# Optimization experiments

Measured on AMD Instinct MI355X. Metric: run time of the kernel, lower is better.

The kernel has to match this reference:

```python
import jax, jax.numpy as jnp
import numpy as np

_LEVELS = jnp.array([-4, -2, -1, 0, 1, 2, 4], dtype=jnp.int32)  # shift-quant 7-value grid 'A'

B, S = 1, 512
IN_F, OUT_F = 4096, 16384
BLOCK = 64
NUM_BLOCKS = (IN_F + BLOCK - 1) // BLOCK  # 64


def setup_inputs() -> dict:
    key = jax.random.key(0)
    k1, k2, k3, k4 = jax.random.split(key, 4)
    x = jax.random.normal(k1, (B, S, IN_F), dtype=jnp.float32)
    idx = jax.random.randint(k2, (OUT_F, IN_F), 0, 7)
    q_weight = _LEVELS[idx]  # int32 values in {-4,-2,-1,0,1,2,4}
    scales = (jax.random.uniform(k3, (OUT_F, NUM_BLOCKS), dtype=jnp.float32) * 0.05 + 0.001).astype(jnp.float16)
    bias = (jax.random.normal(k4, (OUT_F,), dtype=jnp.float32) * 0.02).astype(jnp.float16)
    return {"x": x, "q_weight": q_weight, "scales": scales, "bias": bias, "block_size": BLOCK}


def reference(x, q_weight, scales, bias, block_size):
    # shift_matmul: dequantize blockwise-scaled power-of-two int8 weights, then GEMM.
    out_f, in_f = q_weight.shape
    # broadcast per-block fp16 scales along the in_features axis (handles padding block)
    w_scale = jnp.repeat(scales.astype(jnp.float32), block_size, axis=1)[:, :in_f]  # [out, in]
    w = q_weight.astype(jnp.float32) * w_scale  # [out, in]
    out = jnp.einsum("bsi,oi->bso", x, w)
    out = out + bias.astype(out.dtype)
    return out.astype(x.dtype)
```

## Files before the change

kernel.cpp:

```cpp
#include <hip/hip_runtime.h>
#include <hip/hip_bf16.h>
#include <stdint.h>


#define MM 512
#define NN 16384
#define KK 4096
#define BN 64
#define BK 128
#define NKB (KK / BK)

typedef __bf16 bf16x8 __attribute__((ext_vector_type(8)));
typedef float floatx4 __attribute__((ext_vector_type(4)));

__device__ __forceinline__ void barrier_nodrain() {
    asm volatile("s_waitcnt lgkmcnt(0)\n\ts_barrier" ::: "memory");
}

__device__ __forceinline__ unsigned int pk_bf16_rtn(float lo, float hi) {
    __hip_bfloat162 h = __float22bfloat162_rn(float2{lo, hi});
    return *reinterpret_cast<unsigned int*>(&h);
}

__device__ __forceinline__ uint4 deq8(const int4 q0, const int4 q1, const float s) {
    uint4 u;
    u.x = pk_bf16_rtn((float)q0.x * s, (float)q0.y * s);
    u.y = pk_bf16_rtn((float)q0.z * s, (float)q0.w * s);
    u.z = pk_bf16_rtn((float)q1.x * s, (float)q1.y * s);
    u.w = pk_bf16_rtn((float)q1.z * s, (float)q1.w * s);
    return u;
}

__global__ __launch_bounds__(256) void pack_x(const float* __restrict__ x,
                                              unsigned short* __restrict__ xp) {
    const int t    = blockIdx.x * 256 + threadIdx.x;
    const int lane = t & 63;
    const int mt   = (t >> 6) & 31;
    const int ks   = (t >> 11) & 3;
    const int kb   = t >> 13;
    const int m    = mt * 16 + (lane & 15);
    const int k    = kb * 128 + ks * 32 + (lane >> 4) * 8;
    const float* px = x + (size_t)m * KK + k;
    const float4 a = *(const float4*)px;
    const float4 b = *(const float4*)(px + 4);
    uint4 o;
    o.x = pk_bf16_rtn(a.x, a.y);
    o.y = pk_bf16_rtn(a.z, a.w);
    o.z = pk_bf16_rtn(b.x, b.y);
    o.w = pk_bf16_rtn(b.z, b.w);
    *(uint4*)(xp + (size_t)t * 8) = o;
}

template <bool PRE>
__global__ __launch_bounds__(512, 4) void qlin_gemm(
    const float* __restrict__ xf,
    const unsigned short* __restrict__ xp,
    const int* __restrict__ qw,
    const float* __restrict__ scales,
    const float* __restrict__ bias,
    float* __restrict__ out)
{
    __shared__ unsigned short sB[2][BN * BK];

    const int t    = threadIdx.x;
    const int lane = t & 63;
    const int w    = t >> 6;
    const int ln   = lane & 15;
    const int quad = lane >> 4;
    const int h    = blockIdx.x & 1;
    const int n0   = (blockIdx.x >> 1) * BN;

    const int r    = t >> 4;
    const int oct  = t & 15;
    const int ksp  = oct >> 2;
    const int jp   = r >> 4;
    const int ldst = (((oct & 3) << 4) | (r & 15)) ^ (ksp << 1);
    const int woff = ((ksp * 4 + jp) * 64 + ldst) * 8;
    const int* qp0   = qw + (size_t)(n0 + r) * KK + oct * 8;
    const int* qp1   = qp0 + (size_t)32 * KK;
    const float* sp0 = scales + (size_t)(n0 + r) * 64 + (oct >> 3);
    const float* sp1 = sp0 + 32 * 64;

    floatx4 acc[2][4];
#pragma unroll
    for (int i = 0; i < 2; ++i)
#pragma unroll
        for (int j = 0; j < 4; ++j)
            acc[i][j] = (floatx4)0.0f;

    int4 qa0 = *(const int4*)(qp0);
    int4 qa1 = *(const int4*)(qp0 + 4);
    int4 qb0 = *(const int4*)(qp1);
    int4 qb1 = *(const int4*)(qp1 + 4);
    float sa = sp0[0];
    float sc = sp1[0];

    bf16x8 a[4][2];

    for (int kb = 0; kb < NKB; ++kb) {
        unsigned short* sbuf = sB[kb & 1];

        if constexpr (PRE) {
            const unsigned short* xpb = xp + (size_t)kb * (4 * 32 * 64 * 8);
#pragma unroll
            for (int ks = 0; ks < 4; ++ks) {
                const unsigned short* ap =
                    xpb + (size_t)((ks * 32 + h * 16 + w * 2) * 64 + lane) * 8;
                a[ks][0] = *(const bf16x8*)(ap);
                a[ks][1] = *(const bf16x8*)(ap + 512);
            }
        }

        {
            uint4 u0 = deq8(qa0, qa1, sa);
            uint4 u1 = deq8(qb0, qb1, sc);
            *(uint4*)(sbuf + woff)        = u0;
            *(uint4*)(sbuf + woff + 1024) = u1;
        }

        if (kb + 1 < NKB) {
            qa0 = *(const int4*)(qp0 + (size_t)(kb + 1) * BK);
            qa1 = *(const int4*)(qp0 + (size_t)(kb + 1) * BK + 4);
            qb0 = *(const int4*)(qp1 + (size_t)(kb + 1) * BK);
            qb1 = *(const int4*)(qp1 + (size_t)(kb + 1) * BK + 4);
            sa = sp0[(size_t)(kb + 1) * 2];
            sc = sp1[(size_t)(kb + 1) * 2];
        }

        barrier_nodrain();

#pragma unroll
        for (int ks = 0; ks < 4; ++ks) {
            bf16x8 a0, a1;
            if constexpr (PRE) {
                a0 = a[ks][0];
                a1 = a[ks][1];
            } else {
                const int k = kb * BK + ks * 32 + quad * 8;
#pragma unroll
                for (int i = 0; i < 2; ++i) {
                    const float* px =
                        xf + (size_t)(h * 256 + w * 32 + i * 16 + ln) * KK + k;
                    const float4 f0 = *(const float4*)px;
                    const float4 f1 = *(const float4*)(px + 4);
                    uint4 ua;
                    ua.x = pk_bf16_rtn(f0.x, f0.y);
                    ua.y = pk_bf16_rtn(f0.z, f0.w);
                    ua.z = pk_bf16_rtn(f1.x, f1.y);
                    ua.w = pk_bf16_rtn(f1.z, f1.w);
                    if (i == 0) a0 = *(bf16x8*)&ua; else a1 = *(bf16x8*)&ua;
                }
            }
            const int sl = lane ^ (ks << 1);
#pragma unroll
            for (int jj = 0; jj < 4; jj += 2) {
                bf16x8 b0 = *(const bf16x8*)(sbuf + ((ks * 4 + jj) * 64 + sl) * 8);
                bf16x8 b1 = *(const bf16x8*)(sbuf + ((ks * 4 + jj + 1) * 64 + sl) * 8);
                acc[0][jj]     = __builtin_amdgcn_mfma_f32_16x16x32_bf16(a0, b0, acc[0][jj], 0, 0, 0);
                acc[1][jj]     = __builtin_amdgcn_mfma_f32_16x16x32_bf16(a1, b0, acc[1][jj], 0, 0, 0);
                acc[0][jj + 1] = __builtin_amdgcn_mfma_f32_16x16x32_bf16(a0, b1, acc[0][jj + 1], 0, 0, 0);
                acc[1][jj + 1] = __builtin_amdgcn_mfma_f32_16x16x32_bf16(a1, b1, acc[1][jj + 1], 0, 0, 0);
            }
        }
    }

#pragma unroll
    for (int j = 0; j < 4; ++j) {
        const int n = n0 + j * 16 + ln;
        const float bv = bias[n];
#pragma unroll
        for (int i = 0; i < 2; ++i) {
            const int mbase = h * 256 + w * 32 + i * 16 + quad * 4;
#pragma unroll
            for (int rr = 0; rr < 4; ++rr)
                out[(size_t)(mbase + rr) * NN + n] = acc[i][j][rr] + bv;
        }
    }
}

extern "C" void kernel_launch(void* const* d_in, const int* in_sizes, int n_in,
                              void* d_out, int out_size, void* d_ws, size_t ws_size,
                              hipStream_t stream) {
    const float* x    = (const float*)d_in[0];
    const int* qw     = (const int*)d_in[1];
    const float* scl  = (const float*)d_in[2];
    const float* bias = (const float*)d_in[3];
    float* out        = (float*)d_out;

    dim3 grid(NN / BN * 2);
    dim3 block(512);

    if (ws_size >= (size_t)MM * KK * sizeof(unsigned short)) {
        unsigned short* xp = (unsigned short*)d_ws;
        pack_x<<<dim3(MM * KK / (256 * 8)), dim3(256), 0, stream>>>(x, xp);
        qlin_gemm<true><<<grid, block, 0, stream>>>(x, xp, qw, scl, bias, out);
    } else {
        qlin_gemm<false><<<grid, block, 0, stream>>>(x, nullptr, qw, scl, bias, out);
    }
}
```

Baseline: 442.2 us.

## Software-pipeline dequant, weight prefetch and A loads across K-blocks with per-phase barriers

Restructures the main loop into a prologue-staged ping-pong pipeline. The dequantized weight tile for the next K-block is written while the current tile is consumed, weights are prefetched two blocks ahead, and the A fragments for the next block are loaded right after each phase's MFMAs. Each of the four k-phases now issues all its LDS reads before a barrier and raises wave priority around the MFMA group. The aim is to hide global-load and dequant latency behind matrix math, at the cost of four barriers per K-block instead of one and more registers live at once.

After: 437.4 us. No clear change (-1.1%).

```diff
diff --git a/kernel.cpp b/kernel.cpp
--- a/kernel.cpp
+++ b/kernel.cpp
@@ -97,46 +97,69 @@
 
     bf16x8 a[4][2];
 
+    {
+        uint4 u0 = deq8(qa0, qa1, sa);
+        uint4 u1 = deq8(qb0, qb1, sc);
+        *(uint4*)(sB[0] + woff)        = u0;
+        *(uint4*)(sB[0] + woff + 1024) = u1;
+    }
+    qa0 = *(const int4*)(qp0 + BK);
+    qa1 = *(const int4*)(qp0 + BK + 4);
+    qb0 = *(const int4*)(qp1 + BK);
+    qb1 = *(const int4*)(qp1 + BK + 4);
+    sa = sp0[2];
+    sc = sp1[2];
+    if constexpr (PRE) {
+#pragma unroll
+        for (int p = 0; p < 4; ++p) {
+            const unsigned short* ap =
+                xp + (size_t)((p * 32 + h * 16 + w * 2) * 64 + lane) * 8;
+            a[p][0] = *(const bf16x8*)(ap);
+            a[p][1] = *(const bf16x8*)(ap + 512);
+        }
+    }
+    barrier_nodrain();
+
     for (int kb = 0; kb < NKB; ++kb) {
-        unsigned short* sbuf = sB[kb & 1];
-
-        if constexpr (PRE) {
-            const unsigned short* xpb = xp + (size_t)kb * (4 * 32 * 64 * 8);
-#pragma unroll
-            for (int ks = 0; ks < 4; ++ks) {
-                const unsigned short* ap =
-                    xpb + (size_t)((ks * 32 + h * 16 + w * 2) * 64 + lane) * 8;
-                a[ks][0] = *(const bf16x8*)(ap);
-                a[ks][1] = *(const bf16x8*)(ap + 512);
-            }
-        }
-
-        {
-            uint4 u0 = deq8(qa0, qa1, sa);
-            uint4 u1 = deq8(qb0, qb1, sc);
-            *(uint4*)(sbuf + woff)        = u0;
-            *(uint4*)(sbuf + woff + 1024) = u1;
-        }
-
-        if (kb + 1 < NKB) {
-            qa0 = *(const int4*)(qp0 + (size_t)(kb + 1) * BK);
-            qa1 = *(const int4*)(qp0 + (size_t)(kb + 1) * BK + 4);
-            qb0 = *(const int4*)(qp1 + (size_t)(kb + 1) * BK);
-            qb1 = *(const int4*)(qp1 + (size_t)(kb + 1) * BK + 4);
-            sa = sp0[(size_t)(kb + 1) * 2];
-            sc = sp1[(size_t)(kb + 1) * 2];
-        }
-
-        barrier_nodrain();
-
-#pragma unroll
-        for (int ks = 0; ks < 4; ++ks) {
+        const int cur = kb & 1;
+        const unsigned short* sbR = sB[cur];
+        unsigned short* sbW       = sB[cur ^ 1];
+        const bool stage = (kb + 1 < NKB);
+
+#pragma unroll
+        for (int p = 0; p < 4; ++p) {
+            if (p == 0 && stage) {
+                uint4 u0 = deq8(qa0, qa1, sa);
+                *(uint4*)(sbW + woff) = u0;
+            }
+            if (p == 1 && stage) {
+                uint4 u1 = deq8(qb0, qb1, sc);
+                *(uint4*)(sbW + woff + 1024) = u1;
+            }
+            if (p == 3 && kb + 2 < NKB) {
+                qa0 = *(const int4*)(qp0 + (size_t)(kb + 2) * BK);
+                qa1 = *(const int4*)(qp0 + (size_t)(kb + 2) * BK + 4);
+                qb0 = *(const int4*)(qp1 + (size_t)(kb + 2) * BK);
+                qb1 = *(const int4*)(qp1 + (size_t)(kb + 2) * BK + 4);
+                sa = sp0[(size_t)(kb + 2) * 2];
+                sc = sp1[(size_t)(kb + 2) * 2];
+            }
+
+            const int sl = lane ^ (p << 1);
+            bf16x8 b0 = *(const bf16x8*)(sbR + ((p * 4 + 0) * 64 + sl) * 8);
+            bf16x8 b1 = *(const bf16x8*)(sbR + ((p * 4 + 1) * 64 + sl) * 8);
+            bf16x8 b2 = *(const bf16x8*)(sbR + ((p * 4 + 2) * 64 + sl) * 8);
+            bf16x8 b3 = *(const bf16x8*)(sbR + ((p * 4 + 3) * 64 + sl) * 8);
+
+            barrier_nodrain();
+            __builtin_amdgcn_sched_barrier(0);
+
             bf16x8 a0, a1;
             if constexpr (PRE) {
-                a0 = a[ks][0];
-                a1 = a[ks][1];
+                a0 = a[p][0];
+                a1 = a[p][1];
             } else {
-                const int k = kb * BK + ks * 32 + quad * 8;
+                const int k = kb * BK + p * 32 + quad * 8;
 #pragma unroll
                 for (int i = 0; i < 2; ++i) {
                     const float* px =
@@ -151,15 +174,26 @@
                     if (i == 0) a0 = *(bf16x8*)&ua; else a1 = *(bf16x8*)&ua;
                 }
             }
-            const int sl = lane ^ (ks << 1);
-#pragma unroll
-            for (int jj = 0; jj < 4; jj += 2) {
-                bf16x8 b0 = *(const bf16x8*)(sbuf + ((ks * 4 + jj) * 64 + sl) * 8);
-                bf16x8 b1 = *(const bf16x8*)(sbuf + ((ks * 4 + jj + 1) * 64 + sl) * 8);
-                acc[0][jj]     = __builtin_amdgcn_mfma_f32_16x16x32_bf16(a0, b0, acc[0][jj], 0, 0, 0);
-                acc[1][jj]     = __builtin_amdgcn_mfma_f32_16x16x32_bf16(a1, b0, acc[1][jj], 0, 0, 0);
-                acc[0][jj + 1] = __builtin_amdgcn_mfma_f32_16x16x32_bf16(a0, b1, acc[0][jj + 1], 0, 0, 0);
-                acc[1][jj + 1] = __builtin_amdgcn_mfma_f32_16x16x32_bf16(a1, b1, acc[1][jj + 1], 0, 0, 0);
+
+            __builtin_amdgcn_s_setprio(1);
+            acc[0][0] = __builtin_amdgcn_mfma_f32_16x16x32_bf16(a0, b0, acc[0][0], 0, 0, 0);
+            acc[1][0] = __builtin_amdgcn_mfma_f32_16x16x32_bf16(a1, b0, acc[1][0], 0, 0, 0);
+            acc[0][1] = __builtin_amdgcn_mfma_f32_16x16x32_bf16(a0, b1, acc[0][1], 0, 0, 0);
+            acc[1][1] = __builtin_amdgcn_mfma_f32_16x16x32_bf16(a1, b1, acc[1][1], 0, 0, 0);
+            acc[0][2] = __builtin_amdgcn_mfma_f32_16x16x32_bf16(a0, b2, acc[0][2], 0, 0, 0);
+            acc[1][2] = __builtin_amdgcn_mfma_f32_16x16x32_bf16(a1, b2, acc[1][2], 0, 0, 0);
+            acc[0][3] = __builtin_amdgcn_mfma_f32_16x16x32_bf16(a0, b3, acc[0][3], 0, 0, 0);
+            acc[1][3] = __builtin_amdgcn_mfma_f32_16x16x32_bf16(a1, b3, acc[1][3], 0, 0, 0);
+            __builtin_amdgcn_s_setprio(0);
+
+            if constexpr (PRE) {
+                if (stage) {
+                    const unsigned short* ap =
+                        xp + (size_t)(kb + 1) * (4 * 32 * 64 * 8)
+                           + (size_t)((p * 32 + h * 16 + w * 2) * 64 + lane) * 8;
+                    a[p][0] = *(const bf16x8*)(ap);
+                    a[p][1] = *(const bf16x8*)(ap + 512);
+                }
             }
         }
     }
```

## Pre-dequantize weights to bf16 MFMA layout and stream via global_load_lds

Applied to the files above, without the earlier changes.

Adds a separate pack_w kernel that dequantizes the int32 weights with their scales into bf16, stored in a pre-swizzled per-slab MFMA tile layout in workspace. The GEMM then copies weight tiles straight into shared memory with global_load_lds double buffering, with no in-loop dequant or register staging. In-kernel weight traffic drops from int32 to bf16, and the two M-halves of each slab are now launched far apart in the grid (blockIdx.x>>8). The cost is an extra pass that reads the full int32 weight and writes a 128MB bf16 copy on every call, and a larger workspace requirement. The fallback path is now a naive scalar kernel.

Result: slower. 491.2 us (+11.1%).

```diff
diff --git a/kernel.cpp b/kernel.cpp
--- a/kernel.cpp
+++ b/kernel.cpp
@@ -9,13 +9,10 @@
 #define BN 64
 #define BK 128
 #define NKB (KK / BK)
+#define NSLAB (NN / BN)
 
 typedef __bf16 bf16x8 __attribute__((ext_vector_type(8)));
 typedef float floatx4 __attribute__((ext_vector_type(4)));
-
-__device__ __forceinline__ void barrier_nodrain() {
-    asm volatile("s_waitcnt lgkmcnt(0)\n\ts_barrier" ::: "memory");
-}
 
 __device__ __forceinline__ unsigned int pk_bf16_rtn(float lo, float hi) {
     __hip_bfloat162 h = __float22bfloat162_rn(float2{lo, hi});
@@ -29,6 +26,12 @@
     u.z = pk_bf16_rtn((float)q1.x * s, (float)q1.y * s);
     u.w = pk_bf16_rtn((float)q1.z * s, (float)q1.w * s);
     return u;
+}
+
+__device__ __forceinline__ void gload16(const void* g, void* l) {
+    __builtin_amdgcn_global_load_lds(
+        (const __attribute__((address_space(1))) void*)g,
+        (__attribute__((address_space(3))) void*)l, 16, 0, 0);
 }
 
 __global__ __launch_bounds__(256) void pack_x(const float* __restrict__ x,
@@ -51,12 +54,34 @@
     *(uint4*)(xp + (size_t)t * 8) = o;
 }
 
-template <bool PRE>
+__global__ __launch_bounds__(512) void pack_w(const int* __restrict__ qw,
+                                              const float* __restrict__ scales,
+                                              unsigned short* __restrict__ wb) {
+    const int slab = blockIdx.x >> 5;
+    const int kb   = blockIdx.x & 31;
+    const int u    = threadIdx.x;
+    unsigned short* wt = wb + (size_t)(slab * 32 + kb) * 8192;
+#pragma unroll
+    for (int half = 0; half < 2; ++half) {
+        const int c  = u + half * 512;
+        const int f  = c >> 6;
+        const int l  = c & 63;
+        const int ks = f >> 2;
+        const int j  = f & 3;
+        const int col = slab * 64 + j * 16 + (l & 15);
+        const int k   = kb * 128 + ks * 32 + (l >> 4) * 8;
+        const int* qp = qw + (size_t)col * KK + k;
+        const int4 q0 = *(const int4*)qp;
+        const int4 q1 = *(const int4*)(qp + 4);
+        const float s = scales[(size_t)col * 64 + (k >> 6)];
+        const uint4 uu = deq8(q0, q1, s);
+        *(uint4*)(wt + (size_t)c * 8) = uu;
+    }
+}
+
 __global__ __launch_bounds__(512, 4) void qlin_gemm(
-    const float* __restrict__ xf,
     const unsigned short* __restrict__ xp,
-    const int* __restrict__ qw,
-    const float* __restrict__ scales,
+    const unsigned short* __restrict__ wb,
     const float* __restrict__ bias,
     float* __restrict__ out)
 {
@@ -64,22 +89,14 @@
 
     const int t    = threadIdx.x;
     const int lane = t & 63;
-    const int w    = t >> 6;
+    const int wv   = t >> 6;
     const int ln   = lane & 15;
     const int quad = lane >> 4;
-    const int h    = blockIdx.x & 1;
-    const int n0   = (blockIdx.x >> 1) * BN;
-
-    const int r    = t >> 4;
-    const int oct  = t & 15;
-    const int ksp  = oct >> 2;
-    const int jp   = r >> 4;
-    const int ldst = (((oct & 3) << 4) | (r & 15)) ^ (ksp << 1);
-    const int woff = ((ksp * 4 + jp) * 64 + ldst) * 8;
-    const int* qp0   = qw + (size_t)(n0 + r) * KK + oct * 8;
-    const int* qp1   = qp0 + (size_t)32 * KK;
-    const float* sp0 = scales + (size_t)(n0 + r) * 64 + (oct >> 3);
-    const float* sp1 = sp0 + 32 * 64;
+    const int slab = blockIdx.x & 255;
+    const int h    = blockIdx.x >> 8;
+    const int n0   = slab * BN;
+
+    const unsigned short* wbase = wb + (size_t)slab * 32 * 8192;
 
     floatx4 acc[2][4];
 #pragma unroll
@@ -88,80 +105,48 @@
         for (int j = 0; j < 4; ++j)
             acc[i][j] = (floatx4)0.0f;
 
-    int4 qa0 = *(const int4*)(qp0);
-    int4 qa1 = *(const int4*)(qp0 + 4);
-    int4 qb0 = *(const int4*)(qp1);
-    int4 qb1 = *(const int4*)(qp1 + 4);
-    float sa = sp0[0];
-    float sc = sp1[0];
-
-    bf16x8 a[4][2];
+    {
+        const unsigned short* src = wbase + (size_t)t * 8;
+        gload16(src,            &sB[0][wv * 512]);
+        gload16(src + 512 * 8,  &sB[0][4096 + wv * 512]);
+    }
+    __syncthreads();
 
     for (int kb = 0; kb < NKB; ++kb) {
-        unsigned short* sbuf = sB[kb & 1];
-
-        if constexpr (PRE) {
-            const unsigned short* xpb = xp + (size_t)kb * (4 * 32 * 64 * 8);
-#pragma unroll
-            for (int ks = 0; ks < 4; ++ks) {
-                const unsigned short* ap =
-                    xpb + (size_t)((ks * 32 + h * 16 + w * 2) * 64 + lane) * 8;
-                a[ks][0] = *(const bf16x8*)(ap);
-                a[ks][1] = *(const bf16x8*)(ap + 512);
+        const unsigned short* sb = sB[kb & 1];
+
+        if (kb + 1 < NKB) {
+            const unsigned short* src = wbase + (size_t)(kb + 1) * 8192 + (size_t)t * 8;
+            unsigned short* d0 = &sB[(kb + 1) & 1][wv * 512];
+            unsigned short* d1 = &sB[(kb + 1) & 1][4096 + wv * 512];
+            gload16(src,           d0);
+            gload16(src + 512 * 8, d1);
+        }
+
+        bf16x8 a[4][2];
+#pragma unroll
+        for (int ks = 0; ks < 4; ++ks) {
+            const unsigned short* ap =
+                xp + (size_t)kb * 65536
+                   + (size_t)((ks * 32 + h * 16 + wv * 2) * 64 + lane) * 8;
+            a[ks][0] = *(const bf16x8*)(ap);
+            a[ks][1] = *(const bf16x8*)(ap + 512);
+        }
+
+#pragma unroll
+        for (int ks = 0; ks < 4; ++ks) {
+#pragma unroll
+            for (int jj = 0; jj < 4; jj += 2) {
+                bf16x8 b0 = *(const bf16x8*)(sb + ((ks * 4 + jj) * 64 + lane) * 8);
+                bf16x8 b1 = *(const bf16x8*)(sb + ((ks * 4 + jj + 1) * 64 + lane) * 8);
+                acc[0][jj]     = __builtin_amdgcn_mfma_f32_16x16x32_bf16(a[ks][0], b0, acc[0][jj], 0, 0, 0);
+                acc[1][jj]     = __builtin_amdgcn_mfma_f32_16x16x32_bf16(a[ks][1], b0, acc[1][jj], 0, 0, 0);
+                acc[0][jj + 1] = __builtin_amdgcn_mfma_f32_16x16x32_bf16(a[ks][0], b1, acc[0][jj + 1], 0, 0, 0);
+                acc[1][jj + 1] = __builtin_amdgcn_mfma_f32_16x16x32_bf16(a[ks][1], b1, acc[1][jj + 1], 0, 0, 0);
             }
         }
 
-        {
-            uint4 u0 = deq8(qa0, qa1, sa);
-            uint4 u1 = deq8(qb0, qb1, sc);
-            *(uint4*)(sbuf + woff)        = u0;
-            *(uint4*)(sbuf + woff + 1024) = u1;
-        }
-
-        if (kb + 1 < NKB) {
-            qa0 = *(const int4*)(qp0 + (size_t)(kb + 1) * BK);
-            qa1 = *(const int4*)(qp0 + (size_t)(kb + 1) * BK + 4);
-            qb0 = *(const int4*)(qp1 + (size_t)(kb + 1) * BK);
-            qb1 = *(const int4*)(qp1 + (size_t)(kb + 1) * BK + 4);
-            sa = sp0[(size_t)(kb + 1) * 2];
-            sc = sp1[(size_t)(kb + 1) * 2];
-        }
-
-        barrier_nodrain();
-
-#pragma unroll
-        for (int ks = 0; ks < 4; ++ks) {
-            bf16x8 a0, a1;
-            if constexpr (PRE) {
-                a0 = a[ks][0];
-                a1 = a[ks][1];
-            } else {
-                const int k = kb * BK + ks * 32 + quad * 8;
-#pragma unroll
-                for (int i = 0; i < 2; ++i) {
-                    const float* px =
-                        xf + (size_t)(h * 256 + w * 32 + i * 16 + ln) * KK + k;
-                    const float4 f0 = *(const float4*)px;
-                    const float4 f1 = *(const float4*)(px + 4);
-                    uint4 ua;
-                    ua.x = pk_bf16_rtn(f0.x, f0.y);
-                    ua.y = pk_bf16_rtn(f0.z, f0.w);
-                    ua.z = pk_bf16_rtn(f1.x, f1.y);
-                    ua.w = pk_bf16_rtn(f1.z, f1.w);
-                    if (i == 0) a0 = *(bf16x8*)&ua; else a1 = *(bf16x8*)&ua;
-                }
-            }
-            const int sl = lane ^ (ks << 1);
-#pragma unroll
-            for (int jj = 0; jj < 4; jj += 2) {
-                bf16x8 b0 = *(const bf16x8*)(sbuf + ((ks * 4 + jj) * 64 + sl) * 8);
-                bf16x8 b1 = *(const bf16x8*)(sbuf + ((ks * 4 + jj + 1) * 64 + sl) * 8);
-                acc[0][jj]     = __builtin_amdgcn_mfma_f32_16x16x32_bf16(a0, b0, acc[0][jj], 0, 0, 0);
-                acc[1][jj]     = __builtin_amdgcn_mfma_f32_16x16x32_bf16(a1, b0, acc[1][jj], 0, 0, 0);
-                acc[0][jj + 1] = __builtin_amdgcn_mfma_f32_16x16x32_bf16(a0, b1, acc[0][jj + 1], 0, 0, 0);
-                acc[1][jj + 1] = __builtin_amdgcn_mfma_f32_16x16x32_bf16(a1, b1, acc[1][jj + 1], 0, 0, 0);
-            }
-        }
+        if (kb + 1 < NKB) __syncthreads();
     }
 
 #pragma unroll
@@ -170,12 +155,30 @@
         const float bv = bias[n];
 #pragma unroll
         for (int i = 0; i < 2; ++i) {
-            const int mbase = h * 256 + w * 32 + i * 16 + quad * 4;
+            const int mbase = h * 256 + wv * 32 + i * 16 + quad * 4;
 #pragma unroll
             for (int rr = 0; rr < 4; ++rr)
                 out[(size_t)(mbase + rr) * NN + n] = acc[i][j][rr] + bv;
         }
     }
+}
+
+__global__ __launch_bounds__(256) void qlin_naive(
+    const float* __restrict__ x, const int* __restrict__ qw,
+    const float* __restrict__ scales, const float* __restrict__ bias,
+    float* __restrict__ out) {
+    const int n = blockIdx.x * 256 + threadIdx.x;
+    const int m = blockIdx.y;
+    if (n >= NN || m >= MM) return;
+    float accv = 0.0f;
+    for (int kb = 0; kb < 64; ++kb) {
+        const float s = scales[(size_t)n * 64 + kb];
+        float part = 0.0f;
+        for (int k = kb * 64; k < kb * 64 + 64; ++k)
+            part += x[(size_t)m * KK + k] * (float)qw[(size_t)n * KK + k];
+        accv += part * s;
+    }
+    out[(size_t)m * NN + n] = accv + bias[n];
 }
 
 extern "C" void kernel_launch(void* const* d_in, const int* in_sizes, int n_in,
@@ -187,14 +190,16 @@
     const float* bias = (const float*)d_in[3];
     float* out        = (float*)d_out;
 
-    dim3 grid(NN / BN * 2);
-    dim3 block(512);
-
-    if (ws_size >= (size_t)MM * KK * sizeof(unsigned short)) {
+    const size_t XPB = (size_t)MM * KK * sizeof(unsigned short);
+    const size_t WBB = (size_t)NN * KK * sizeof(unsigned short);
+
+    if (ws_size >= XPB + WBB) {
         unsigned short* xp = (unsigned short*)d_ws;
+        unsigned short* wb = (unsigned short*)((char*)d_ws + XPB);
         pack_x<<<dim3(MM * KK / (256 * 8)), dim3(256), 0, stream>>>(x, xp);
-        qlin_gemm<true><<<grid, block, 0, stream>>>(x, xp, qw, scl, bias, out);
+        pack_w<<<dim3(NSLAB * 32), dim3(512), 0, stream>>>(qw, scl, wb);
+        qlin_gemm<<<dim3(NSLAB * 2), dim3(512), 0, stream>>>(xp, wb, bias, out);
     } else {
-        qlin_gemm<false><<<grid, block, 0, stream>>>(x, nullptr, qw, scl, bias, out);
-    }
-}
+        qlin_naive<<<dim3(NN / 256, MM), dim3(256), 0, stream>>>(x, qw, scl, bias, out);
+    }
+}
```
